# Kernel tuning notes

Hardware: AMD Instinct MI355X
Metric: run time of the kernel (lower is better)

The kernel has to match this reference:

```python
import jax, jax.numpy as jnp
import numpy as np

N_NODES = 50000
N_EDGES = 1000000
F = 256          # feature_size
NC = 300         # n_content_dims
ED = 64          # embedding_dim = 2**int(log2(F/4))
L = 3            # n_layers


def setup_inputs() -> dict:
    key = jax.random.key(0)
    ks = jax.random.split(key, 20)
    s = 0.05  # weight init scale
    return {
        'node_ids': jnp.arange(N_NODES, dtype=jnp.int32),
        'content': jax.random.normal(ks[0], (N_NODES, NC), jnp.float32),
        'src': jax.random.randint(ks[1], (N_EDGES,), 0, N_NODES, jnp.int32),
        'dst': jax.random.randint(ks[2], (N_EDGES,), 0, N_NODES, jnp.int32),
        'emb': jax.random.normal(ks[3], (N_NODES + 1, ED), jnp.float32) / ED,
        'W_exp': jax.random.normal(ks[4], (F, ED), jnp.float32) * s,
        'b_exp': jnp.zeros((F,), jnp.float32),
        'W_p1': jax.random.normal(ks[5], (NC, NC), jnp.float32) * s,
        'b_p1': jnp.zeros((NC,), jnp.float32),
        'W_p2': jax.random.normal(ks[6], (F, NC), jnp.float32) * s,
        'b_p2': jnp.zeros((F,), jnp.float32),
        'W_conv': jax.random.normal(ks[7], (L, F, 2 * F), jnp.float32) * s,
        'b_conv': jnp.zeros((L, F), jnp.float32),
        'Wo1': jax.random.normal(ks[8], (L - 1, F, F), jnp.float32) * s,
        'bo1': jnp.zeros((L - 1, F), jnp.float32),
        'Wo2': jax.random.normal(ks[9], (L - 1, F, F), jnp.float32) * s,
        'bo2': jnp.zeros((L - 1, F), jnp.float32),
    }


def _lrelu(x):
    return jax.nn.leaky_relu(x, 0.1)


def reference(node_ids, content, src, dst, emb, W_exp, b_exp, W_p1, b_p1,
              W_p2, b_p2, W_conv, b_conv, Wo1, bo1, Wo2, bo2):
    # initial node repr: expansion(node_emb) + proj(content)  (GaussianNoise = identity at eval)
    h = _lrelu(emb[node_ids] @ W_exp.T + b_exp)                 # [N, F]
    c = _lrelu(content @ W_p1.T + b_p1)
    c = _lrelu(c @ W_p2.T + b_p2)
    h = h + c

    ones = jnp.ones((src.shape[0],), h.dtype)
    deg = jax.ops.segment_sum(ones, dst, num_segments=N_NODES)  # in-degree
    w = (deg + 1.0)[:, None]                                    # +1 for self-loop

    for i in range(L):
        # message passing: sum neighbor h (with self-loop), then neighbor mean
        agg = jax.ops.segment_sum(h[src], dst, num_segments=N_NODES) + h  # [N, F]
        h_agg = (agg - h) / jnp.maximum(w - 1.0, 1.0)
        h_concat = jnp.concatenate([h, h_agg], axis=1)          # [N, 2F]
        h_new = h_concat @ W_conv[i].T + b_conv[i]
        if i < L - 1:
            h_new = _lrelu(h_new)
        # L2-normalize rows
        h_new = h_new / jnp.maximum(
            jnp.linalg.norm(h_new, axis=1, keepdims=True), 1e-6)
        if i < L - 1:  # W_out block (non-prediction layers)
            h_new = _lrelu(h_new @ Wo1[i].T + bo1[i])
            h_new = h_new @ Wo2[i].T + bo2[i]
        h = h_new
    return h
```

## Files before the change

### kernel.cpp

```cpp
#include <hip/hip_runtime.h>
#include <stdint.h>

#define NNODES 50000
#define NROWS_PAD 50048
#define NEDGES 1000000
#define FD 256
#define NCPAD 384
#define EDIM 64
#define NSCAN ((NNODES + 255) / 256)

typedef unsigned short u16;
typedef __attribute__((ext_vector_type(8))) short short8;
typedef __attribute__((ext_vector_type(4))) float floatx4;

__device__ __forceinline__ float bf2f(u16 x) {
    union { unsigned u; float f; } c; c.u = ((unsigned)x) << 16; return c.f;
}
__device__ __forceinline__ u16 f2bf(float f) {
    union { float f; unsigned u; } c; c.f = f;
    unsigned u = c.u;
    return (u16)((u + 0x7fffu + ((u >> 16) & 1u)) >> 16);
}
__device__ __forceinline__ void gload16(const u16* g, u16* l) {
    __builtin_amdgcn_global_load_lds(
        (const __attribute__((address_space(1))) void*)g,
        (__attribute__((address_space(3))) void*)l, 16, 0, 0);
}

__global__ void detect_kernel(const u16* p, int* flag) {
    __shared__ int smax;
    if (threadIdx.x == 0) smax = 0;
    __syncthreads();
    int m = 0;
    for (int i = threadIdx.x; i < 8192; i += 256) {
        int e = (p[i] >> 7) & 0xFF;
        m = m > e ? m : e;
    }
    atomicMax(&smax, m);
    __syncthreads();
    if (threadIdx.x == 0) *flag = (smax >= 140) ? 1 : 0;
}

#define NB_CONV 1798
#define NB_CNT4 489
#define PREP_GRID (NB_CONV + NB_CNT4)
__global__ __launch_bounds__(512) void prep_kernel(
    u16* arena, const int* flagp,
    const void* wexp, const void* bexp, const void* wp1, const void* bp1,
    const void* wp2, const void* bp2, const void* wconv, const void* bconv,
    const void* wo1, const void* bo1, const void* wo2, const void* bo2,
    const int* dst, int* deg)
{
    const int bid = blockIdx.x;
    if (bid >= NB_CONV) {
        int q4 = (bid - NB_CONV) * 512 + threadIdx.x;
        if (q4 * 4 + 3 < NEDGES) {
            int4 d = *(const int4*)(dst + q4 * 4);
            atomicAdd(&deg[d.x], 1);
            atomicAdd(&deg[d.y], 1);
            atomicAdd(&deg[d.z], 1);
            atomicAdd(&deg[d.w], 1);
        }
        return;
    }
    const int offs[13]  = {0,16384,16640,164096,164480,262784,263040,
                           656256,657024,788096,788608,919680,920192};
    const int rreal[12] = {256,1,300,1,256,1,768,1,512,1,512,1};
    const int creal[12] = {64,256,300,300,300,256,512,768,256,512,256,512};
    const int cpd[12]   = {64,256,384,384,384,256,512,768,256,512,256,512};
    long gid = (long)bid * 512 + threadIdx.x;
    if (gid >= 920192) return;
    const void* srcs[12] = {wexp,bexp,wp1,bp1,wp2,bp2,wconv,bconv,wo1,bo1,wo2,bo2};
    int fl = *flagp;
    int t = 0;
    #pragma unroll
    for (int i = 1; i < 12; ++i) if (gid >= offs[i]) t = i;
    long local = gid - offs[t];
    int rr = (int)(local / cpd[t]);
    int cc = (int)(local % cpd[t]);
    u16 v = 0;
    if (rr < rreal[t] && cc < creal[t]) {
        long si = (long)rr * creal[t] + cc;
        v = fl ? f2bf(((const float*)srcs[t])[si]) : ((const u16*)srcs[t])[si];
    }
    arena[gid] = v;
}

__global__ __launch_bounds__(256) void scan1_kernel(const int* deg, int* bsum) {
    __shared__ int s[256];
    int t = threadIdx.x;
    int i = blockIdx.x * 256 + t;
    s[t] = (i < NNODES) ? deg[i] : 0;
    __syncthreads();
    #pragma unroll
    for (int off = 128; off > 0; off >>= 1) {
        if (t < off) s[t] += s[t + off];
        __syncthreads();
    }
    if (t == 0) bsum[blockIdx.x] = s[0];
}

__global__ __launch_bounds__(256) void scan2_kernel(int* bsum, int* row_start) {
    __shared__ int s[256];
    int t = threadIdx.x;
    int v = (t < NSCAN) ? bsum[t] : 0;
    s[t] = v;
    __syncthreads();
    for (int off = 1; off < 256; off <<= 1) {
        int x = (t >= off) ? s[t - off] : 0;
        __syncthreads();
        s[t] += x;
        __syncthreads();
    }
    if (t < NSCAN) bsum[t] = s[t] - v;
    if (t == 0) row_start[NNODES] = NEDGES;
}

__global__ __launch_bounds__(256) void scan3_kernel(const int* deg, const int* bsum,
        int* row_start, int* cursor, float* inv_w) {
    __shared__ int s[256];
    int t = threadIdx.x;
    int i = blockIdx.x * 256 + t;
    int v = (i < NNODES) ? deg[i] : 0;
    s[t] = v;
    __syncthreads();
    for (int off = 1; off < 256; off <<= 1) {
        int x = (t >= off) ? s[t - off] : 0;
        __syncthreads();
        s[t] += x;
        __syncthreads();
    }
    if (i < NNODES) {
        int base = bsum[blockIdx.x] + s[t] - v;
        row_start[i] = base;
        cursor[i] = base;
        inv_w[i] = 1.0f / (float)(v > 0 ? v : 1);
    }
}

#define IF_GRID (391 * 7)
__global__ __launch_bounds__(512, 4) void initfill_kernel(
    const void* __restrict__ content, const void* __restrict__ emb,
    const int* __restrict__ flagp,
    const u16* __restrict__ Wp1, const u16* __restrict__ bp1,
    const u16* __restrict__ Wp2, const u16* __restrict__ bp2,
    const u16* __restrict__ Wexp, const u16* __restrict__ bexp,
    u16* __restrict__ hbuf,
    const int* __restrict__ src, const int* __restrict__ dst,
    int* __restrict__ cursor, int* __restrict__ esrc)
{
    __shared__ __align__(16) u16 sA[64 * 64];
    __shared__ __align__(16) u16 sB[384 * 32];
    __shared__ __align__(16) u16 T[64 * 384];

    const int g7 = blockIdx.x / 7, r7 = blockIdx.x % 7;
    if (r7 >= 2) {
        int fb = g7 * 5 + (r7 - 2);
        int e = fb * 512 + threadIdx.x;
        if (e < NEDGES) {
            int v = dst[e];
            int pos = atomicAdd(&cursor[v], 1);
            if ((unsigned)pos < (unsigned)NEDGES) esrc[pos] = src[e];
        }
        return;
    }
    const int bm = (g7 * 2 + r7) * 64;
    const int t = threadIdx.x;
    const int wave = t >> 6, lane = t & 63;
    const int quad = lane >> 4, l16 = lane & 15;
    const int wm = wave >> 2, wn = wave & 3;
    const int lrow = lane >> 2, lcol = (lane & 3) * 8;
    const int fl = *flagp;

    {
        int row = t >> 3;
        int c0 = (t & 7) * 8;
        int gm = bm + row;
        u16 o[8];
        if (gm < NNODES) {
            if (fl) {
                const float* ep = (const float*)emb + (size_t)gm * EDIM + c0;
                float4 x = *(const float4*)ep;
                float4 y = *(const float4*)(ep + 4);
                o[0]=f2bf(x.x); o[1]=f2bf(x.y); o[2]=f2bf(x.z); o[3]=f2bf(x.w);
                o[4]=f2bf(y.x); o[5]=f2bf(y.y); o[6]=f2bf(y.z); o[7]=f2bf(y.w);
            } else {
                const u16* ep = (const u16*)emb + (size_t)gm * EDIM + c0;
                ushort4 x = *(const ushort4*)ep;
                ushort4 y = *(const ushort4*)(ep + 4);
                o[0]=x.x; o[1]=x.y; o[2]=x.z; o[3]=x.w;
                o[4]=y.x; o[5]=y.y; o[6]=y.z; o[7]=y.w;
            }
        } else {
            #pragma unroll
            for (int k = 0; k < 8; ++k) o[k] = 0;
        }
        u16* d = &sA[(row * 64 + c0) ^ ((row & 7) << 3)];
        #pragma unroll
        for (int k = 0; k < 8; ++k) d[k] = o[k];
    }
    #pragma unroll
    for (int j = 0; j < 6; ++j) {
        int idx = (j * 512 + t) * 8;
        int row = idx / 384;
        int c0 = idx % 384;
        int gm = bm + row;
        u16 o[8];
        if (gm < NNODES && c0 + 8 <= 300) {
            if (fl) {
                const float* cp = (const float*)content + (size_t)gm * 300 + c0;
                float4 x = *(const float4*)cp;
                float4 y = *(const float4*)(cp + 4);
                o[0]=f2bf(x.x); o[1]=f2bf(x.y); o[2]=f2bf(x.z); o[3]=f2bf(x.w);
                o[4]=f2bf(y.x); o[5]=f2bf(y.y); o[6]=f2bf(y.z); o[7]=f2bf(y.w);
            } else {
                const u16* cp = (const u16*)content + (size_t)gm * 300 + c0;
                ushort4 x = *(const ushort4*)cp;
                ushort4 y = *(const ushort4*)(cp + 4);
                o[0]=x.x; o[1]=x.y; o[2]=x.z; o[3]=x.w;
                o[4]=y.x; o[5]=y.y; o[6]=y.z; o[7]=y.w;
            }
        } else if (gm < NNODES && c0 < 300) {
            #pragma unroll
            for (int k = 0; k < 8; ++k) {
                int c = c0 + k;
                o[k] = (c < 300)
                    ? (fl ? f2bf(((const float*)content)[(size_t)gm * 300 + c])
                          : ((const u16*)content)[(size_t)gm * 300 + c])
                    : (u16)0;
            }
        } else {
            #pragma unroll
            for (int k = 0; k < 8; ++k) o[k] = 0;
        }
        u16* d = &T[(row * 384 + c0) ^ ((row & 7) << 3)];
        #pragma unroll
        for (int k = 0; k < 8; ++k) d[k] = o[k];
    }
    __syncthreads();

    floatx4 a1[2][6];
    #pragma unroll
    for (int i = 0; i < 2; ++i)
        #pragma unroll
        for (int j = 0; j < 6; ++j) a1[i][j] = (floatx4){0.f, 0.f, 0.f, 0.f};
    for (int kt = 0; kt < 384; kt += 32) {
        #pragma unroll
        for (int c = 0; c < 3; ++c) {
            int r0 = wave * 48 + c * 16;
            gload16(Wp1 + (size_t)(r0 + lrow) * NCPAD + kt + lcol, &sB[r0 * 32]);
        }
        __syncthreads();
        short8 af[2];
        #pragma unroll
        for (int mt = 0; mt < 2; ++mt) {
            int row = wm * 32 + mt * 16 + l16;
            af[mt] = *(const short8*)&T[(row * 384 + kt + quad * 8) ^ ((row & 7) << 3)];
        }
        #pragma unroll
        for (int nt = 0; nt < 6; ++nt) {
            short8 bf = *(const short8*)&sB[(wn * 96 + nt * 16 + l16) * 32 + quad * 8];
            a1[0][nt] = __builtin_amdgcn_mfma_f32_16x16x32_bf16(af[0], bf, a1[0][nt], 0, 0, 0);
            a1[1][nt] = __builtin_amdgcn_mfma_f32_16x16x32_bf16(af[1], bf, a1[1][nt], 0, 0, 0);
        }
        __syncthreads();
    }
    #pragma unroll
    for (int nt = 0; nt < 6; ++nt) {
        int col = wn * 96 + nt * 16 + l16;
        float bv = bf2f(bp1[col]);
        #pragma unroll
        for (int mt = 0; mt < 2; ++mt)
            #pragma unroll
            for (int rr = 0; rr < 4; ++rr) {
                int row = wm * 32 + mt * 16 + quad * 4 + rr;
                float v = a1[mt][nt][rr] + bv;
                v = v > 0.f ? v : 0.1f * v;
                T[(row * NCPAD + col) ^ ((row & 7) << 3)] = f2bf(v);
            }
    }
    __syncthreads();

    floatx4 a2[2][4];
    #pragma unroll
    for (int i = 0; i < 2; ++i)
        #pragma unroll
        for (int j = 0; j < 4; ++j) a2[i][j] = (floatx4){0.f, 0.f, 0.f, 0.f};
    for (int kt = 0; kt < 384; kt += 32) {
        #pragma unroll
        for (int c = 0; c < 2; ++c) {
            int r0 = wave * 32 + c * 16;
            gload16(Wp2 + (size_t)(r0 + lrow) * NCPAD + kt + lcol, &sB[r0 * 32]);
        }
        __syncthreads();
        short8 af[2];
        #pragma unroll
        for (int mt = 0; mt < 2; ++mt) {
            int row = wm * 32 + mt * 16 + l16;
            af[mt] = *(const short8*)&T[(row * NCPAD + kt + quad * 8) ^ ((row & 7) << 3)];
        }
        #pragma unroll
        for (int nt = 0; nt < 4; ++nt) {
            short8 bf = *(const short8*)&sB[(wn * 64 + nt * 16 + l16) * 32 + quad * 8];
            a2[0][nt] = __builtin_amdgcn_mfma_f32_16x16x32_bf16(af[0], bf, a2[0][nt], 0, 0, 0);
            a2[1][nt] = __builtin_amdgcn_mfma_f32_16x16x32_bf16(af[1], bf, a2[1][nt], 0, 0, 0);
        }
        __syncthreads();
    }

    floatx4 aE[2][4];
    #pragma unroll
    for (int i = 0; i < 2; ++i)
        #pragma unroll
        for (int j = 0; j < 4; ++j) aE[i][j] = (floatx4){0.f, 0.f, 0.f, 0.f};
    for (int kt = 0; kt < 64; kt += 32) {
        #pragma unroll
        for (int c = 0; c < 2; ++c) {
            int r0 = wave * 32 + c * 16;
            gload16(Wexp + (size_t)(r0 + lrow) * EDIM + kt + lcol, &sB[r0 * 32]);
        }
        __syncthreads();
        short8 af[2];
        #pragma unroll
        for (int mt = 0; mt < 2; ++mt) {
            int row = wm * 32 + mt * 16 + l16;
            af[mt] = *(const short8*)&sA[(row * 64 + kt + quad * 8) ^ ((row & 7) << 3)];
        }
        #pragma unroll
        for (int nt = 0; nt < 4; ++nt) {
            short8 bf = *(const short8*)&sB[(wn * 64 + nt * 16 + l16) * 32 + quad * 8];
            aE[0][nt] = __builtin_amdgcn_mfma_f32_16x16x32_bf16(af[0], bf, aE[0][nt], 0, 0, 0);
            aE[1][nt] = __builtin_amdgcn_mfma_f32_16x16x32_bf16(af[1], bf, aE[1][nt], 0, 0, 0);
        }
        __syncthreads();
    }

    #pragma unroll
    for (int nt = 0; nt < 4; ++nt) {
        int col = wn * 64 + nt * 16 + l16;
        float bE = bf2f(bexp[col]), b2 = bf2f(bp2[col]);
        #pragma unroll
        for (int mt = 0; mt < 2; ++mt)
            #pragma unroll
            for (int rr = 0; rr < 4; ++rr) {
                int row = wm * 32 + mt * 16 + quad * 4 + rr;
                int gm = bm + row;
                if (gm < NNODES) {
                    float hE = aE[mt][nt][rr] + bE; hE = hE > 0.f ? hE : 0.1f * hE;
                    float c2 = a2[mt][nt][rr] + b2; c2 = c2 > 0.f ? c2 : 0.1f * c2;
                    hbuf[(size_t)gm * FD + col] = f2bf(hE + c2);
                }
            }
    }
}

__global__ __launch_bounds__(512, 4) void layer_kernel(
    const u16* __restrict__ h, const u16* __restrict__ agg,
    const u16* __restrict__ Wc, const u16* __restrict__ bc,
    const u16* __restrict__ W1, const u16* __restrict__ b1,
    const u16* __restrict__ W2, const u16* __restrict__ b2,
    u16* __restrict__ out)
{
    __shared__ __align__(16) u16 sA[2][64 * 32];
    __shared__ __align__(16) u16 sB[2][256 * 32];
    __shared__ __align__(16) u16 T[64 * 256];
    __shared__ float ssq[4][64];

    const int t = threadIdx.x;
    const int wave = t >> 6, lane = t & 63;
    const int quad = lane >> 4, l16 = lane & 15;
    const int wm = wave >> 2, wn = wave & 3;
    const int lrow = lane >> 2, lcol = (lane & 3) * 8;
    const int bm = blockIdx.x * 64;

    floatx4 acc[2][4];
    #pragma unroll
    for (int i = 0; i < 2; ++i)
        #pragma unroll
        for (int j = 0; j < 4; ++j) acc[i][j] = (floatx4){0.f, 0.f, 0.f, 0.f};

    for (int kt = 0; kt < 512; kt += 64) {
        const u16* Ap = (kt < 256) ? h : agg;
        const int kk = kt & 255;
        {
            int hh = wave & 1, r0 = (wave >> 1) * 16;
            gload16(Ap + (size_t)(bm + r0 + lrow) * 256 + kk + hh * 32 + lcol,
                    &sA[hh][r0 * 32]);
        }
        #pragma unroll
        for (int c = 0; c < 4; ++c) {
            int hh = c >> 1, r0 = wave * 32 + (c & 1) * 16;
            gload16(Wc + (size_t)(r0 + lrow) * 512 + kt + hh * 32 + lcol,
                    &sB[hh][r0 * 32]);
        }
        __syncthreads();
        #pragma unroll
        for (int g = 0; g < 2; ++g) {
            short8 af[2], bf[4];
            #pragma unroll
            for (int mt = 0; mt < 2; ++mt)
                af[mt] = *(const short8*)&sA[g][(wm * 32 + mt * 16 + l16) * 32 + quad * 8];
            #pragma unroll
            for (int nt = 0; nt < 4; ++nt)
                bf[nt] = *(const short8*)&sB[g][(wn * 64 + nt * 16 + l16) * 32 + quad * 8];
            #pragma unroll
            for (int mt = 0; mt < 2; ++mt)
                #pragma unroll
                for (int nt = 0; nt < 4; ++nt)
                    acc[mt][nt] = __builtin_amdgcn_mfma_f32_16x16x32_bf16(af[mt], bf[nt], acc[mt][nt], 0, 0, 0);
        }
        __syncthreads();
    }
    {
        float part[2][4];
        #pragma unroll
        for (int mt = 0; mt < 2; ++mt)
            #pragma unroll
            for (int rr = 0; rr < 4; ++rr) part[mt][rr] = 0.f;
        #pragma unroll
        for (int nt = 0; nt < 4; ++nt) {
            float bv = bf2f(bc[wn * 64 + nt * 16 + l16]);
            #pragma unroll
            for (int mt = 0; mt < 2; ++mt)
                #pragma unroll
                for (int rr = 0; rr < 4; ++rr) {
                    float v = acc[mt][nt][rr] + bv;
                    v = v > 0.f ? v : 0.1f * v;
                    part[mt][rr] += v * v;
                }
        }
        #pragma unroll
        for (int off = 1; off < 16; off <<= 1)
            #pragma unroll
            for (int mt = 0; mt < 2; ++mt)
                #pragma unroll
                for (int rr = 0; rr < 4; ++rr)
                    part[mt][rr] += __shfl_xor(part[mt][rr], off);
        if (l16 == 0)
            #pragma unroll
            for (int mt = 0; mt < 2; ++mt)
                #pragma unroll
                for (int rr = 0; rr < 4; ++rr)
                    ssq[wn][wm * 32 + mt * 16 + quad * 4 + rr] = part[mt][rr];
        __syncthreads();
        #pragma unroll
        for (int mt = 0; mt < 2; ++mt)
            #pragma unroll
            for (int rr = 0; rr < 4; ++rr) {
                int row = wm * 32 + mt * 16 + quad * 4 + rr;
                float s = 1.0f / fmaxf(sqrtf(ssq[0][row] + ssq[1][row] +
                                             ssq[2][row] + ssq[3][row]), 1e-6f);
                #pragma unroll
                for (int nt = 0; nt < 4; ++nt) {
                    int col = wn * 64 + nt * 16 + l16;
                    float v = acc[mt][nt][rr] + bf2f(bc[col]);
                    v = v > 0.f ? v : 0.1f * v;
                    T[(row * 256 + col) ^ ((row & 7) << 3)] = f2bf(v * s);
                }
            }
        __syncthreads();
    }

    #pragma unroll
    for (int i = 0; i < 2; ++i)
        #pragma unroll
        for (int j = 0; j < 4; ++j) acc[i][j] = (floatx4){0.f, 0.f, 0.f, 0.f};
    for (int kt = 0; kt < 256; kt += 64) {
        #pragma unroll
        for (int c = 0; c < 4; ++c) {
            int hh = c >> 1, r0 = wave * 32 + (c & 1) * 16;
            gload16(W1 + (size_t)(r0 + lrow) * 256 + kt + hh * 32 + lcol,
                    &sB[hh][r0 * 32]);
        }
        __syncthreads();
        #pragma unroll
        for (int g = 0; g < 2; ++g) {
            short8 af[2], bf[4];
            #pragma unroll
            for (int mt = 0; mt < 2; ++mt) {
                int row = wm * 32 + mt * 16 + l16;
                af[mt] = *(const short8*)&T[(row * 256 + kt + g * 32 + quad * 8) ^ ((row & 7) << 3)];
            }
            #pragma unroll
            for (int nt = 0; nt < 4; ++nt)
                bf[nt] = *(const short8*)&sB[g][(wn * 64 + nt * 16 + l16) * 32 + quad * 8];
            #pragma unroll
            for (int mt = 0; mt < 2; ++mt)
                #pragma unroll
                for (int nt = 0; nt < 4; ++nt)
                    acc[mt][nt] = __builtin_amdgcn_mfma_f32_16x16x32_bf16(af[mt], bf[nt], acc[mt][nt], 0, 0, 0);
        }
        __syncthreads();
    }
    #pragma unroll
    for (int nt = 0; nt < 4; ++nt) {
        int col = wn * 64 + nt * 16 + l16;
        float bv = bf2f(b1[col]);
        #pragma unroll
        for (int mt = 0; mt < 2; ++mt) {
            #pragma unroll
            for (int r = 0; r < 4; ++r) {
                int row = wm * 32 + mt * 16 + quad * 4 + r;
                float v = acc[mt][nt][r] + bv;
                v = v > 0.f ? v : 0.1f * v;
                T[(row * 256 + col) ^ ((row & 7) << 3)] = f2bf(v);
            }
        }
    }
    __syncthreads();

    #pragma unroll
    for (int i = 0; i < 2; ++i)
        #pragma unroll
        for (int j = 0; j < 4; ++j) acc[i][j] = (floatx4){0.f, 0.f, 0.f, 0.f};
    for (int kt = 0; kt < 256; kt += 64) {
        #pragma unroll
        for (int c = 0; c < 4; ++c) {
            int hh = c >> 1, r0 = wave * 32 + (c & 1) * 16;
            gload16(W2 + (size_t)(r0 + lrow) * 256 + kt + hh * 32 + lcol,
                    &sB[hh][r0 * 32]);
        }
        __syncthreads();
        #pragma unroll
        for (int g = 0; g < 2; ++g) {
            short8 af[2], bf[4];
            #pragma unroll
            for (int mt = 0; mt < 2; ++mt) {
                int row = wm * 32 + mt * 16 + l16;
                af[mt] = *(const short8*)&T[(row * 256 + kt + g * 32 + quad * 8) ^ ((row & 7) << 3)];
            }
            #pragma unroll
            for (int nt = 0; nt < 4; ++nt)
                bf[nt] = *(const short8*)&sB[g][(wn * 64 + nt * 16 + l16) * 32 + quad * 8];
            #pragma unroll
            for (int mt = 0; mt < 2; ++mt)
                #pragma unroll
                for (int nt = 0; nt < 4; ++nt)
                    acc[mt][nt] = __builtin_amdgcn_mfma_f32_16x16x32_bf16(af[mt], bf[nt], acc[mt][nt], 0, 0, 0);
        }
        __syncthreads();
    }
    #pragma unroll
    for (int nt = 0; nt < 4; ++nt) {
        int col = wn * 64 + nt * 16 + l16;
        float bv = bf2f(b2[col]);
        #pragma unroll
        for (int mt = 0; mt < 2; ++mt) {
            #pragma unroll
            for (int r = 0; r < 4; ++r) {
                int row = wm * 32 + mt * 16 + quad * 4 + r;
                int gm = bm + row;
                if (gm < NNODES) {
                    float v = acc[mt][nt][r] + bv;
                    out[(size_t)gm * 256 + col] = f2bf(v);
                }
            }
        }
    }
}

__global__ __launch_bounds__(512, 4) void final_kernel(
    const u16* __restrict__ h, const u16* __restrict__ agg,
    const u16* __restrict__ Wc, const u16* __restrict__ bc,
    float* __restrict__ out)
{
    __shared__ __align__(16) u16 sA[2][64 * 32];
    __shared__ __align__(16) u16 sB[2][256 * 32];
    __shared__ float ssq[4][64];

    const int t = threadIdx.x;
    const int wave = t >> 6, lane = t & 63;
    const int quad = lane >> 4, l16 = lane & 15;
    const int wm = wave >> 2, wn = wave & 3;
    const int lrow = lane >> 2, lcol = (lane & 3) * 8;
    const int bm = blockIdx.x * 64;

    floatx4 acc[2][4];
    #pragma unroll
    for (int i = 0; i < 2; ++i)
        #pragma unroll
        for (int j = 0; j < 4; ++j) acc[i][j] = (floatx4){0.f, 0.f, 0.f, 0.f};

    for (int kt = 0; kt < 512; kt += 64) {
        const u16* Ap = (kt < 256) ? h : agg;
        const int kk = kt & 255;
        {
            int hh = wave & 1, r0 = (wave >> 1) * 16;
            gload16(Ap + (size_t)(bm + r0 + lrow) * 256 + kk + hh * 32 + lcol,
                    &sA[hh][r0 * 32]);
        }
        #pragma unroll
        for (int c = 0; c < 4; ++c) {
            int hh = c >> 1, r0 = wave * 32 + (c & 1) * 16;
            gload16(Wc + (size_t)(r0 + lrow) * 512 + kt + hh * 32 + lcol,
                    &sB[hh][r0 * 32]);
        }
        __syncthreads();
        #pragma unroll
        for (int g = 0; g < 2; ++g) {
            short8 af[2], bf[4];
            #pragma unroll
            for (int mt = 0; mt < 2; ++mt)
                af[mt] = *(const short8*)&sA[g][(wm * 32 + mt * 16 + l16) * 32 + quad * 8];
            #pragma unroll
            for (int nt = 0; nt < 4; ++nt)
                bf[nt] = *(const short8*)&sB[g][(wn * 64 + nt * 16 + l16) * 32 + quad * 8];
            #pragma unroll
            for (int mt = 0; mt < 2; ++mt)
                #pragma unroll
                for (int nt = 0; nt < 4; ++nt)
                    acc[mt][nt] = __builtin_amdgcn_mfma_f32_16x16x32_bf16(af[mt], bf[nt], acc[mt][nt], 0, 0, 0);
        }
        __syncthreads();
    }
    float part[2][4];
    #pragma unroll
    for (int mt = 0; mt < 2; ++mt)
        #pragma unroll
        for (int rr = 0; rr < 4; ++rr) part[mt][rr] = 0.f;
    #pragma unroll
    for (int nt = 0; nt < 4; ++nt) {
        float bv = bf2f(bc[wn * 64 + nt * 16 + l16]);
        #pragma unroll
        for (int mt = 0; mt < 2; ++mt)
            #pragma unroll
            for (int rr = 0; rr < 4; ++rr) {
                float v = acc[mt][nt][rr] + bv;
                part[mt][rr] += v * v;
            }
    }
    #pragma unroll
    for (int off = 1; off < 16; off <<= 1)
        #pragma unroll
        for (int mt = 0; mt < 2; ++mt)
            #pragma unroll
            for (int rr = 0; rr < 4; ++rr)
                part[mt][rr] += __shfl_xor(part[mt][rr], off);
    if (l16 == 0)
        #pragma unroll
        for (int mt = 0; mt < 2; ++mt)
            #pragma unroll
            for (int rr = 0; rr < 4; ++rr)
                ssq[wn][wm * 32 + mt * 16 + quad * 4 + rr] = part[mt][rr];
    __syncthreads();
    #pragma unroll
    for (int mt = 0; mt < 2; ++mt)
        #pragma unroll
        for (int rr = 0; rr < 4; ++rr) {
            int row = wm * 32 + mt * 16 + quad * 4 + rr;
            int gm = bm + row;
            float s = 1.0f / fmaxf(sqrtf(ssq[0][row] + ssq[1][row] +
                                         ssq[2][row] + ssq[3][row]), 1e-6f);
            if (gm < NNODES) {
                #pragma unroll
                for (int nt = 0; nt < 4; ++nt) {
                    int col = wn * 64 + nt * 16 + l16;
                    out[(size_t)gm * 256 + col] = (acc[mt][nt][rr] + bf2f(bc[col])) * s;
                }
            }
        }
}

__global__ __launch_bounds__(256) void agg_kernel(
    const u16* h, const int* row_start, const int* esrc,
    const float* inv_w, u16* out)
{
    int gid = blockIdx.x * blockDim.x + threadIdx.x;
    int wid = gid >> 6;
    int lane = gid & 63;
    if (wid >= NNODES) return;
    int e0 = row_start[wid], e1 = row_start[wid + 1];
    e0 = max(0, min(e0, NEDGES));
    e1 = max(e0, min(e1, NEDGES));
    float a0 = 0.f, a1 = 0.f, a2 = 0.f, a3 = 0.f;
    int e = e0;
    for (; e + 4 <= e1; e += 4) {
        int u0 = esrc[e + 0]; if ((unsigned)u0 >= (unsigned)NNODES) u0 = 0;
        int u1 = esrc[e + 1]; if ((unsigned)u1 >= (unsigned)NNODES) u1 = 0;
        int u2 = esrc[e + 2]; if ((unsigned)u2 >= (unsigned)NNODES) u2 = 0;
        int u3 = esrc[e + 3]; if ((unsigned)u3 >= (unsigned)NNODES) u3 = 0;
        ushort4 t0 = *(const ushort4*)(h + (size_t)u0 * FD + lane * 4);
        ushort4 t1 = *(const ushort4*)(h + (size_t)u1 * FD + lane * 4);
        ushort4 t2 = *(const ushort4*)(h + (size_t)u2 * FD + lane * 4);
        ushort4 t3 = *(const ushort4*)(h + (size_t)u3 * FD + lane * 4);
        a0 += bf2f(t0.x) + bf2f(t1.x) + bf2f(t2.x) + bf2f(t3.x);
        a1 += bf2f(t0.y) + bf2f(t1.y) + bf2f(t2.y) + bf2f(t3.y);
        a2 += bf2f(t0.z) + bf2f(t1.z) + bf2f(t2.z) + bf2f(t3.z);
        a3 += bf2f(t0.w) + bf2f(t1.w) + bf2f(t2.w) + bf2f(t3.w);
    }
    for (; e < e1; ++e) {
        int u = esrc[e];
        if ((unsigned)u >= (unsigned)NNODES) u = 0;
        ushort4 tv = *(const ushort4*)(h + (size_t)u * FD + lane * 4);
        a0 += bf2f(tv.x); a1 += bf2f(tv.y); a2 += bf2f(tv.z); a3 += bf2f(tv.w);
    }
    float s = inv_w[wid];
    ushort4 ov;
    ov.x = f2bf(a0 * s); ov.y = f2bf(a1 * s); ov.z = f2bf(a2 * s); ov.w = f2bf(a3 * s);
    *(ushort4*)(out + (size_t)wid * FD + lane * 4) = ov;
}

extern "C" void kernel_launch(void* const* d_in, const int* in_sizes, int n_in,
                              void* d_out, int out_size, void* d_ws, size_t ws_size,
                              hipStream_t stream) {
    const void* content = d_in[1];
    const int* src      = (const int*)d_in[2];
    const int* dst      = (const int*)d_in[3];
    const void* emb     = d_in[4];

    char* ws = (char*)d_ws;
    u16* arena = (u16*)(ws);
    u16* hbuf  = (u16*)(ws + 1840640);
    u16* buf2  = (u16*)(ws + 27465216);
    int*   deg    = (int*)(ws + 78714368);
    int*   rs     = (int*)(ws + 78914560);
    int*   cursor = (int*)(ws + 79114752);
    float* inv_w  = (float*)(ws + 79314944);
    int*   esrc   = (int*)(ws + 79515136);
    int*   bsum   = (int*)(ws + 83515648);
    int*   flag   = (int*)(ws + 83516672);

    u16* aWexp  = arena;            u16* aBexp  = arena + 16384;
    u16* aWp1   = arena + 16640;    u16* aBp1   = arena + 164096;
    u16* aWp2   = arena + 164480;   u16* aBp2   = arena + 262784;
    u16* aWconv = arena + 263040;   u16* aBconv = arena + 656256;
    u16* aWo1   = arena + 657024;   u16* aBo1   = arena + 788096;
    u16* aWo2   = arena + 788608;   u16* aBo2   = arena + 919680;

    const int MB64 = NROWS_PAD / 64;

    detect_kernel<<<1, 256, 0, stream>>>((const u16*)content, flag);
    hipMemsetAsync(deg, 0, (size_t)NNODES * 4, stream);
    prep_kernel<<<PREP_GRID, 512, 0, stream>>>(arena, flag,
        d_in[5], d_in[6], d_in[7], d_in[8], d_in[9], d_in[10], d_in[11],
        d_in[12], d_in[13], d_in[14], d_in[15], d_in[16], dst, deg);

    scan1_kernel<<<NSCAN, 256, 0, stream>>>(deg, bsum);
    scan2_kernel<<<1, 256, 0, stream>>>(bsum, rs);
    scan3_kernel<<<NSCAN, 256, 0, stream>>>(deg, bsum, rs, cursor, inv_w);

    initfill_kernel<<<IF_GRID, 512, 0, stream>>>(content, emb, flag,
        aWp1, aBp1, aWp2, aBp2, aWexp, aBexp, hbuf, src, dst, cursor, esrc);

    for (int i = 0; i < 3; ++i) {
        agg_kernel<<<(NNODES * 64) / 256, 256, 0, stream>>>(hbuf, rs, esrc, inv_w, buf2);
        if (i < 2) {
            layer_kernel<<<dim3(MB64), dim3(512), 0, stream>>>(
                hbuf, buf2,
                aWconv + (size_t)i * FD * 2 * FD, aBconv + (size_t)i * FD,
                aWo1 + (size_t)i * FD * FD, aBo1 + (size_t)i * FD,
                aWo2 + (size_t)i * FD * FD, aBo2 + (size_t)i * FD,
                hbuf);
        } else {
            final_kernel<<<dim3(MB64), dim3(512), 0, stream>>>(
                hbuf, buf2,
                aWconv + (size_t)i * FD * 2 * FD, aBconv + (size_t)i * FD,
                (float*)d_out);
        }
    }
}
```

Before: 655.5 us.

## Fuse neighbor aggregation into layer GEMM kernels with ping-pong h buffers

Removes the separate agg_kernel. Each layer kernel now gathers and averages its 64 rows' neighbor features into LDS, then feeds them straight to the MFMA GEMM in place of reading an aggregated buffer from global memory. Two h buffers alternate between layers so a gather never reads rows being overwritten by the same launch. The initfill edge-scatter path is also vectorised to handle four edges per thread, and the grid is rebalanced. The risk is lower occupancy from the added LDS and latency-bound gathers now running inside the GEMM blocks, with only 782 blocks to hide that latency.

```diff
diff --git a/kernel.cpp b/kernel.cpp
--- a/kernel.cpp
+++ b/kernel.cpp
@@ -53,9 +53,9 @@
 {
     const int bid = blockIdx.x;
     if (bid >= NB_CONV) {
-        int q4 = (bid - NB_CONV) * 512 + threadIdx.x;
-        if (q4 * 4 + 3 < NEDGES) {
-            int4 d = *(const int4*)(dst + q4 * 4);
+        int base = ((bid - NB_CONV) * 512 + threadIdx.x) * 4;
+        if (base < NEDGES) {
+            int4 d = *(const int4*)(dst + base);
             atomicAdd(&deg[d.x], 1);
             atomicAdd(&deg[d.y], 1);
             atomicAdd(&deg[d.z], 1);
@@ -138,7 +138,7 @@
     }
 }
 
-#define IF_GRID (391 * 7)
+#define IF_GRID (98 * 13)
 __global__ __launch_bounds__(512, 4) void initfill_kernel(
     const void* __restrict__ content, const void* __restrict__ emb,
     const int* __restrict__ flagp,
@@ -153,18 +153,28 @@
     __shared__ __align__(16) u16 sB[384 * 32];
     __shared__ __align__(16) u16 T[64 * 384];
 
-    const int g7 = blockIdx.x / 7, r7 = blockIdx.x % 7;
-    if (r7 >= 2) {
-        int fb = g7 * 5 + (r7 - 2);
-        int e = fb * 512 + threadIdx.x;
-        if (e < NEDGES) {
-            int v = dst[e];
-            int pos = atomicAdd(&cursor[v], 1);
-            if ((unsigned)pos < (unsigned)NEDGES) esrc[pos] = src[e];
+    const int g13 = blockIdx.x / 13, r13 = blockIdx.x % 13;
+    if (r13 >= 8) {
+        int fb = g13 * 5 + (r13 - 8);
+        if (fb >= NB_CNT4) return;
+        int base = (fb * 512 + threadIdx.x) * 4;
+        if (base < NEDGES) {
+            int4 s4 = *(const int4*)(src + base);
+            int4 d4 = *(const int4*)(dst + base);
+            int p0 = atomicAdd(&cursor[d4.x], 1);
+            int p1 = atomicAdd(&cursor[d4.y], 1);
+            int p2 = atomicAdd(&cursor[d4.z], 1);
+            int p3 = atomicAdd(&cursor[d4.w], 1);
+            if ((unsigned)p0 < (unsigned)NEDGES) esrc[p0] = s4.x;
+            if ((unsigned)p1 < (unsigned)NEDGES) esrc[p1] = s4.y;
+            if ((unsigned)p2 < (unsigned)NEDGES) esrc[p2] = s4.z;
+            if ((unsigned)p3 < (unsigned)NEDGES) esrc[p3] = s4.w;
         }
         return;
     }
-    const int bm = (g7 * 2 + r7) * 64;
+    const int iid = g13 * 8 + r13;
+    if (iid >= 782) return;
+    const int bm = iid * 64;
     const int t = threadIdx.x;
     const int wave = t >> 6, lane = t & 63;
     const int quad = lane >> 4, l16 = lane & 15;
@@ -196,8 +206,8 @@
             for (int k = 0; k < 8; ++k) o[k] = 0;
         }
         u16* d = &sA[(row * 64 + c0) ^ ((row & 7) << 3)];
-        #pragma unroll
-        for (int k = 0; k < 8; ++k) d[k] = o[k];
+        *(ushort4*)d = (ushort4){o[0], o[1], o[2], o[3]};
+        *(ushort4*)(d + 4) = (ushort4){o[4], o[5], o[6], o[7]};
     }
     #pragma unroll
     for (int j = 0; j < 6; ++j) {
@@ -234,8 +244,8 @@
             for (int k = 0; k < 8; ++k) o[k] = 0;
         }
         u16* d = &T[(row * 384 + c0) ^ ((row & 7) << 3)];
-        #pragma unroll
-        for (int k = 0; k < 8; ++k) d[k] = o[k];
+        *(ushort4*)d = (ushort4){o[0], o[1], o[2], o[3]};
+        *(ushort4*)(d + 4) = (ushort4){o[4], o[5], o[6], o[7]};
     }
     __syncthreads();
 
@@ -354,8 +364,9 @@
     }
 }
 
-__global__ __launch_bounds__(512, 4) void layer_kernel(
-    const u16* __restrict__ h, const u16* __restrict__ agg,
+__global__ __launch_bounds__(512, 4) void flayer_kernel(
+    const u16* __restrict__ h, const int* __restrict__ rs,
+    const int* __restrict__ esrc, const float* __restrict__ inv_w,
     const u16* __restrict__ Wc, const u16* __restrict__ bc,
     const u16* __restrict__ W1, const u16* __restrict__ b1,
     const u16* __restrict__ W2, const u16* __restrict__ b2,
@@ -363,7 +374,7 @@
 {
     __shared__ __align__(16) u16 sA[2][64 * 32];
     __shared__ __align__(16) u16 sB[2][256 * 32];
-    __shared__ __align__(16) u16 T[64 * 256];
+    __shared__ __align__(16) u16 GT[64 * 256];
     __shared__ float ssq[4][64];
 
     const int t = threadIdx.x;
@@ -373,18 +384,55 @@
     const int lrow = lane >> 2, lcol = (lane & 3) * 8;
     const int bm = blockIdx.x * 64;
 
+    #pragma unroll 1
+    for (int i = 0; i < 8; ++i) {
+        int row = wave * 8 + i;
+        int gm = bm + row;
+        float a0 = 0.f, a1 = 0.f, a2 = 0.f, a3 = 0.f;
+        if (gm < NNODES) {
+            int e0 = rs[gm], e1 = rs[gm + 1];
+            e0 = max(0, min(e0, NEDGES));
+            e1 = max(e0, min(e1, NEDGES));
+            int e = e0;
+            for (; e + 4 <= e1; e += 4) {
+                int u0 = esrc[e + 0]; if ((unsigned)u0 >= (unsigned)NNODES) u0 = 0;
+                int u1 = esrc[e + 1]; if ((unsigned)u1 >= (unsigned)NNODES) u1 = 0;
+                int u2 = esrc[e + 2]; if ((unsigned)u2 >= (unsigned)NNODES) u2 = 0;
+                int u3 = esrc[e + 3]; if ((unsigned)u3 >= (unsigned)NNODES) u3 = 0;
+                ushort4 t0 = *(const ushort4*)(h + (size_t)u0 * FD + lane * 4);
+                ushort4 t1 = *(const ushort4*)(h + (size_t)u1 * FD + lane * 4);
+                ushort4 t2 = *(const ushort4*)(h + (size_t)u2 * FD + lane * 4);
+                ushort4 t3 = *(const ushort4*)(h + (size_t)u3 * FD + lane * 4);
+                a0 += bf2f(t0.x) + bf2f(t1.x) + bf2f(t2.x) + bf2f(t3.x);
+                a1 += bf2f(t0.y) + bf2f(t1.y) + bf2f(t2.y) + bf2f(t3.y);
+                a2 += bf2f(t0.z) + bf2f(t1.z) + bf2f(t2.z) + bf2f(t3.z);
+                a3 += bf2f(t0.w) + bf2f(t1.w) + bf2f(t2.w) + bf2f(t3.w);
+            }
+            for (; e < e1; ++e) {
+                int u = esrc[e];
+                if ((unsigned)u >= (unsigned)NNODES) u = 0;
+                ushort4 tv = *(const ushort4*)(h + (size_t)u * FD + lane * 4);
+                a0 += bf2f(tv.x); a1 += bf2f(tv.y); a2 += bf2f(tv.z); a3 += bf2f(tv.w);
+            }
+            float s = inv_w[gm];
+            a0 *= s; a1 *= s; a2 *= s; a3 *= s;
+        }
+        ushort4 ov;
+        ov.x = f2bf(a0); ov.y = f2bf(a1); ov.z = f2bf(a2); ov.w = f2bf(a3);
+        *(ushort4*)&GT[(row * 256 + lane * 4) ^ ((row & 7) << 3)] = ov;
+    }
+    __syncthreads();
+
     floatx4 acc[2][4];
     #pragma unroll
     for (int i = 0; i < 2; ++i)
         #pragma unroll
         for (int j = 0; j < 4; ++j) acc[i][j] = (floatx4){0.f, 0.f, 0.f, 0.f};
 
-    for (int kt = 0; kt < 512; kt += 64) {
-        const u16* Ap = (kt < 256) ? h : agg;
-        const int kk = kt & 255;
+    for (int kt = 0; kt < 256; kt += 64) {
         {
             int hh = wave & 1, r0 = (wave >> 1) * 16;
-            gload16(Ap + (size_t)(bm + r0 + lrow) * 256 + kk + hh * 32 + lcol,
+            gload16(h + (size_t)(bm + r0 + lrow) * 256 + kt + hh * 32 + lcol,
                     &sA[hh][r0 * 32]);
         }
         #pragma unroll
@@ -400,6 +448,33 @@
             #pragma unroll
             for (int mt = 0; mt < 2; ++mt)
                 af[mt] = *(const short8*)&sA[g][(wm * 32 + mt * 16 + l16) * 32 + quad * 8];
+            #pragma unroll
+            for (int nt = 0; nt < 4; ++nt)
+                bf[nt] = *(const short8*)&sB[g][(wn * 64 + nt * 16 + l16) * 32 + quad * 8];
+            #pragma unroll
+            for (int mt = 0; mt < 2; ++mt)
+                #pragma unroll
+                for (int nt = 0; nt < 4; ++nt)
+                    acc[mt][nt] = __builtin_amdgcn_mfma_f32_16x16x32_bf16(af[mt], bf[nt], acc[mt][nt], 0, 0, 0);
+        }
+        __syncthreads();
+    }
+    for (int kt = 256; kt < 512; kt += 64) {
+        #pragma unroll
+        for (int c = 0; c < 4; ++c) {
+            int hh = c >> 1, r0 = wave * 32 + (c & 1) * 16;
+            gload16(Wc + (size_t)(r0 + lrow) * 512 + kt + hh * 32 + lcol,
+                    &sB[hh][r0 * 32]);
+        }
+        __syncthreads();
+        #pragma unroll
+        for (int g = 0; g < 2; ++g) {
+            short8 af[2], bf[4];
+            #pragma unroll
+            for (int mt = 0; mt < 2; ++mt) {
+                int row = wm * 32 + mt * 16 + l16;
+                af[mt] = *(const short8*)&GT[(row * 256 + (kt - 256) + g * 32 + quad * 8) ^ ((row & 7) << 3)];
+            }
             #pragma unroll
             for (int nt = 0; nt < 4; ++nt)
                 bf[nt] = *(const short8*)&sB[g][(wn * 64 + nt * 16 + l16) * 32 + quad * 8];
@@ -455,7 +530,7 @@
                     int col = wn * 64 + nt * 16 + l16;
                     float v = acc[mt][nt][rr] + bf2f(bc[col]);
                     v = v > 0.f ? v : 0.1f * v;
-                    T[(row * 256 + col) ^ ((row & 7) << 3)] = f2bf(v * s);
+                    GT[(row * 256 + col) ^ ((row & 7) << 3)] = f2bf(v * s);
                 }
             }
         __syncthreads();
@@ -479,7 +554,7 @@
             #pragma unroll
             for (int mt = 0; mt < 2; ++mt) {
                 int row = wm * 32 + mt * 16 + l16;
-                af[mt] = *(const short8*)&T[(row * 256 + kt + g * 32 + quad * 8) ^ ((row & 7) << 3)];
+                af[mt] = *(const short8*)&GT[(row * 256 + kt + g * 32 + quad * 8) ^ ((row & 7) << 3)];
             }
             #pragma unroll
             for (int nt = 0; nt < 4; ++nt)
@@ -503,7 +578,7 @@
                 int row = wm * 32 + mt * 16 + quad * 4 + r;
                 float v = acc[mt][nt][r] + bv;
                 v = v > 0.f ? v : 0.1f * v;
-                T[(row * 256 + col) ^ ((row & 7) << 3)] = f2bf(v);
+                GT[(row * 256 + col) ^ ((row & 7) << 3)] = f2bf(v);
             }
         }
     }
@@ -527,7 +602,7 @@
             #pragma unroll
             for (int mt = 0; mt < 2; ++mt) {
                 int row = wm * 32 + mt * 16 + l16;
-                af[mt] = *(const short8*)&T[(row * 256 + kt + g * 32 + quad * 8) ^ ((row & 7) << 3)];
+                af[mt] = *(const short8*)&GT[(row * 256 + kt + g * 32 + quad * 8) ^ ((row & 7) << 3)];
             }
             #pragma unroll
             for (int nt = 0; nt < 4; ++nt)
@@ -559,13 +634,15 @@
     }
 }
 
-__global__ __launch_bounds__(512, 4) void final_kernel(
-    const u16* __restrict__ h, const u16* __restrict__ agg,
+__global__ __launch_bounds__(512, 4) void ffinal_kernel(
+    const u16* __restrict__ h, const int* __restrict__ rs,
+    const int* __restrict__ esrc, const float* __restrict__ inv_w,
     const u16* __restrict__ Wc, const u16* __restrict__ bc,
     float* __restrict__ out)
 {
     __shared__ __align__(16) u16 sA[2][64 * 32];
     __shared__ __align__(16) u16 sB[2][256 * 32];
+    __shared__ __align__(16) u16 GT[64 * 256];
     __shared__ float ssq[4][64];
 
     const int t = threadIdx.x;
@@ -575,18 +652,55 @@
     const int lrow = lane >> 2, lcol = (lane & 3) * 8;
     const int bm = blockIdx.x * 64;
 
+    #pragma unroll 1
+    for (int i = 0; i < 8; ++i) {
+        int row = wave * 8 + i;
+        int gm = bm + row;
+        float a0 = 0.f, a1 = 0.f, a2 = 0.f, a3 = 0.f;
+        if (gm < NNODES) {
+            int e0 = rs[gm], e1 = rs[gm + 1];
+            e0 = max(0, min(e0, NEDGES));
+            e1 = max(e0, min(e1, NEDGES));
+            int e = e0;
+            for (; e + 4 <= e1; e += 4) {
+                int u0 = esrc[e + 0]; if ((unsigned)u0 >= (unsigned)NNODES) u0 = 0;
+                int u1 = esrc[e + 1]; if ((unsigned)u1 >= (unsigned)NNODES) u1 = 0;
+                int u2 = esrc[e + 2]; if ((unsigned)u2 >= (unsigned)NNODES) u2 = 0;
+                int u3 = esrc[e + 3]; if ((unsigned)u3 >= (unsigned)NNODES) u3 = 0;
+                ushort4 t0 = *(const ushort4*)(h + (size_t)u0 * FD + lane * 4);
+                ushort4 t1 = *(const ushort4*)(h + (size_t)u1 * FD + lane * 4);
+                ushort4 t2 = *(const ushort4*)(h + (size_t)u2 * FD + lane * 4);
+                ushort4 t3 = *(const ushort4*)(h + (size_t)u3 * FD + lane * 4);
+                a0 += bf2f(t0.x) + bf2f(t1.x) + bf2f(t2.x) + bf2f(t3.x);
+                a1 += bf2f(t0.y) + bf2f(t1.y) + bf2f(t2.y) + bf2f(t3.y);
+                a2 += bf2f(t0.z) + bf2f(t1.z) + bf2f(t2.z) + bf2f(t3.z);
+                a3 += bf2f(t0.w) + bf2f(t1.w) + bf2f(t2.w) + bf2f(t3.w);
+            }
+            for (; e < e1; ++e) {
+                int u = esrc[e];
+                if ((unsigned)u >= (unsigned)NNODES) u = 0;
+                ushort4 tv = *(const ushort4*)(h + (size_t)u * FD + lane * 4);
+                a0 += bf2f(tv.x); a1 += bf2f(tv.y); a2 += bf2f(tv.z); a3 += bf2f(tv.w);
+            }
+            float s = inv_w[gm];
+            a0 *= s; a1 *= s; a2 *= s; a3 *= s;
+        }
+        ushort4 ov;
+        ov.x = f2bf(a0); ov.y = f2bf(a1); ov.z = f2bf(a2); ov.w = f2bf(a3);
+        *(ushort4*)&GT[(row * 256 + lane * 4) ^ ((row & 7) << 3)] = ov;
+    }
+    __syncthreads();
+
     floatx4 acc[2][4];
     #pragma unroll
     for (int i = 0; i < 2; ++i)
         #pragma unroll
         for (int j = 0; j < 4; ++j) acc[i][j] = (floatx4){0.f, 0.f, 0.f, 0.f};
 
-    for (int kt = 0; kt < 512; kt += 64) {
-        const u16* Ap = (kt < 256) ? h : agg;
-        const int kk = kt & 255;
+    for (int kt = 0; kt < 256; kt += 64) {
         {
             int hh = wave & 1, r0 = (wave >> 1) * 16;
-            gload16(Ap + (size_t)(bm + r0 + lrow) * 256 + kk + hh * 32 + lcol,
+            gload16(h + (size_t)(bm + r0 + lrow) * 256 + kt + hh * 32 + lcol,
                     &sA[hh][r0 * 32]);
         }
         #pragma unroll
@@ -602,6 +716,33 @@
             #pragma unroll
             for (int mt = 0; mt < 2; ++mt)
                 af[mt] = *(const short8*)&sA[g][(wm * 32 + mt * 16 + l16) * 32 + quad * 8];
+            #pragma unroll
+            for (int nt = 0; nt < 4; ++nt)
+                bf[nt] = *(const short8*)&sB[g][(wn * 64 + nt * 16 + l16) * 32 + quad * 8];
+            #pragma unroll
+            for (int mt = 0; mt < 2; ++mt)
+                #pragma unroll
+                for (int nt = 0; nt < 4; ++nt)
+                    acc[mt][nt] = __builtin_amdgcn_mfma_f32_16x16x32_bf16(af[mt], bf[nt], acc[mt][nt], 0, 0, 0);
+        }
+        __syncthreads();
+    }
+    for (int kt = 256; kt < 512; kt += 64) {
+        #pragma unroll
+        for (int c = 0; c < 4; ++c) {
+            int hh = c >> 1, r0 = wave * 32 + (c & 1) * 16;
+            gload16(Wc + (size_t)(r0 + lrow) * 512 + kt + hh * 32 + lcol,
+                    &sB[hh][r0 * 32]);
+        }
+        __syncthreads();
+        #pragma unroll
+        for (int g = 0; g < 2; ++g) {
+            short8 af[2], bf[4];
+            #pragma unroll
+            for (int mt = 0; mt < 2; ++mt) {
+                int row = wm * 32 + mt * 16 + l16;
+                af[mt] = *(const short8*)&GT[(row * 256 + (kt - 256) + g * 32 + quad * 8) ^ ((row & 7) << 3)];
+            }
             #pragma unroll
             for (int nt = 0; nt < 4; ++nt)
                 bf[nt] = *(const short8*)&sB[g][(wn * 64 + nt * 16 + l16) * 32 + quad * 8];
@@ -659,45 +800,6 @@
                 }
             }
         }
-}
-
-__global__ __launch_bounds__(256) void agg_kernel(
-    const u16* h, const int* row_start, const int* esrc,
-    const float* inv_w, u16* out)
-{
-    int gid = blockIdx.x * blockDim.x + threadIdx.x;
-    int wid = gid >> 6;
-    int lane = gid & 63;
-    if (wid >= NNODES) return;
-    int e0 = row_start[wid], e1 = row_start[wid + 1];
-    e0 = max(0, min(e0, NEDGES));
-    e1 = max(e0, min(e1, NEDGES));
-    float a0 = 0.f, a1 = 0.f, a2 = 0.f, a3 = 0.f;
-    int e = e0;
-    for (; e + 4 <= e1; e += 4) {
-        int u0 = esrc[e + 0]; if ((unsigned)u0 >= (unsigned)NNODES) u0 = 0;
-        int u1 = esrc[e + 1]; if ((unsigned)u1 >= (unsigned)NNODES) u1 = 0;
-        int u2 = esrc[e + 2]; if ((unsigned)u2 >= (unsigned)NNODES) u2 = 0;
-        int u3 = esrc[e + 3]; if ((unsigned)u3 >= (unsigned)NNODES) u3 = 0;
-        ushort4 t0 = *(const ushort4*)(h + (size_t)u0 * FD + lane * 4);
-        ushort4 t1 = *(const ushort4*)(h + (size_t)u1 * FD + lane * 4);
-        ushort4 t2 = *(const ushort4*)(h + (size_t)u2 * FD + lane * 4);
-        ushort4 t3 = *(const ushort4*)(h + (size_t)u3 * FD + lane * 4);
-        a0 += bf2f(t0.x) + bf2f(t1.x) + bf2f(t2.x) + bf2f(t3.x);
-        a1 += bf2f(t0.y) + bf2f(t1.y) + bf2f(t2.y) + bf2f(t3.y);
-        a2 += bf2f(t0.z) + bf2f(t1.z) + bf2f(t2.z) + bf2f(t3.z);
-        a3 += bf2f(t0.w) + bf2f(t1.w) + bf2f(t2.w) + bf2f(t3.w);
-    }
-    for (; e < e1; ++e) {
-        int u = esrc[e];
-        if ((unsigned)u >= (unsigned)NNODES) u = 0;
-        ushort4 tv = *(const ushort4*)(h + (size_t)u * FD + lane * 4);
-        a0 += bf2f(tv.x); a1 += bf2f(tv.y); a2 += bf2f(tv.z); a3 += bf2f(tv.w);
-    }
-    float s = inv_w[wid];
-    ushort4 ov;
-    ov.x = f2bf(a0 * s); ov.y = f2bf(a1 * s); ov.z = f2bf(a2 * s); ov.w = f2bf(a3 * s);
-    *(ushort4*)(out + (size_t)wid * FD + lane * 4) = ov;
 }
 
 extern "C" void kernel_launch(void* const* d_in, const int* in_sizes, int n_in,
@@ -710,8 +812,8 @@
 
     char* ws = (char*)d_ws;
     u16* arena = (u16*)(ws);
-    u16* hbuf  = (u16*)(ws + 1840640);
-    u16* buf2  = (u16*)(ws + 27465216);
+    u16* hbufA = (u16*)(ws + 1840640);
+    u16* hbufB = (u16*)(ws + 27465216);
     int*   deg    = (int*)(ws + 78714368);
     int*   rs     = (int*)(ws + 78914560);
     int*   cursor = (int*)(ws + 79114752);
@@ -740,22 +842,14 @@
     scan3_kernel<<<NSCAN, 256, 0, stream>>>(deg, bsum, rs, cursor, inv_w);
 
     initfill_kernel<<<IF_GRID, 512, 0, stream>>>(content, emb, flag,
-        aWp1, aBp1, aWp2, aBp2, aWexp, aBexp, hbuf, src, dst, cursor, esrc);
-
-    for (int i = 0; i < 3; ++i) {
-        agg_kernel<<<(NNODES * 64) / 256, 256, 0, stream>>>(hbuf, rs, esrc, inv_w, buf2);
-        if (i < 2) {
-            layer_kernel<<<dim3(MB64), dim3(512), 0, stream>>>(
-                hbuf, buf2,
-                aWconv + (size_t)i * FD * 2 * FD, aBconv + (size_t)i * FD,
-                aWo1 + (size_t)i * FD * FD, aBo1 + (size_t)i * FD,
-                aWo2 + (size_t)i * FD * FD, aBo2 + (size_t)i * FD,
-                hbuf);
-        } else {
-            final_kernel<<<dim3(MB64), dim3(512), 0, stream>>>(
-                hbuf, buf2,
-                aWconv + (size_t)i * FD * 2 * FD, aBconv + (size_t)i * FD,
-                (float*)d_out);
-        }
-    }
-}
+        aWp1, aBp1, aWp2, aBp2, aWexp, aBexp, hbufA, src, dst, cursor, esrc);
+
+    flayer_kernel<<<MB64, 512, 0, stream>>>(hbufA, rs, esrc, inv_w,
+        aWconv, aBconv, aWo1, aBo1, aWo2, aBo2, hbufB);
+    flayer_kernel<<<MB64, 512, 0, stream>>>(hbufB, rs, esrc, inv_w,
+        aWconv + (size_t)1 * FD * 2 * FD, aBconv + FD,
+        aWo1 + (size_t)1 * FD * FD, aBo1 + FD,
+        aWo2 + (size_t)1 * FD * FD, aBo2 + FD, hbufA);
+    ffinal_kernel<<<MB64, 512, 0, stream>>>(hbufA, rs, esrc, inv_w,
+        aWconv + (size_t)2 * FD * 2 * FD, aBconv + 2 * FD, (float*)d_out);
+}
```

New measurement: 723.6 us. +10.4%, slower.
